# Kernel tuning notes

Measured on AMD Instinct MI355X. Metric: run time of the kernel, lower is better.

Reference implementation:

```python
import jax, jax.numpy as jnp
import numpy as np
import math

N_HEAD = 16
STRIDE = 128
C = 8


def _sparse_causal_mask(q_len, k_len):
    # Mirrors LingLongAttention._sparse_causal_mask (static, host-side numpy).
    cols = np.arange(k_len)
    rows = np.arange(k_len)[:, None]
    strided = (cols % STRIDE) >= (STRIDE - C)          # last C cols of each stride block
    local = (cols[None, :] // STRIDE) == (rows // STRIDE)  # same stride block as query
    causal = cols[None, :] <= rows
    layout = (strided[None, :] | local) & causal       # [k_len, k_len]
    return jnp.asarray(layout[k_len - q_len:])         # [q_len, k_len]


def setup_inputs() -> dict:
    key = jax.random.key(0)
    k1, k2, k3 = jax.random.split(key, 3)
    B, S, E = 2, 2048, 1024
    return {
        "hidden_states": jax.random.normal(k1, (B, S, E), dtype=jnp.float32),
        "W_attn": jax.random.normal(k2, (E, 3 * E), dtype=jnp.float32) * 0.02,
        "b_attn": jnp.zeros((3 * E,), dtype=jnp.float32),
        "W_proj": jax.random.normal(k3, (E, E), dtype=jnp.float32) * 0.02,
        "b_proj": jnp.zeros((E,), dtype=jnp.float32),
    }


def reference(hidden_states, W_attn, b_attn, W_proj, b_proj):
    B, S, E = hidden_states.shape
    H = N_HEAD
    D = E // H
    # Conv1D: x @ W + b, then split into q,k,v
    qkv = hidden_states @ W_attn + b_attn                 # [B,S,3E]
    q, k, v = jnp.split(qkv, 3, axis=-1)
    split = lambda t: t.reshape(B, S, H, D).transpose(0, 2, 1, 3)  # [B,H,S,D]
    q, k, v = split(q), split(k), split(v)
    scale = jnp.asarray(1.0 / math.sqrt(D), dtype=q.dtype)
    scores = jnp.einsum("bhqd,bhkd->bhqk", q, k) * scale  # [B,H,S,S]
    mask = _sparse_causal_mask(S, S)[None, None]          # [1,1,S,S]
    mask_value = jnp.asarray(jnp.finfo(scores.dtype).min, dtype=scores.dtype)
    scores = jnp.where(mask, scores, mask_value)
    attn = jax.nn.softmax(scores, axis=-1)
    out = jnp.einsum("bhqk,bhkd->bhqd", attn, v)          # [B,H,S,D]
    out = out.transpose(0, 2, 1, 3).reshape(B, S, E)      # merge heads
    return out @ W_proj + b_proj
```

## Files before the change

### kernel.cpp

```cpp
#include <hip/hip_runtime.h>
#include <hip/hip_bf16.h>
#include <stdint.h>

typedef unsigned short u16;
typedef uint32_t u32;
typedef short s16x8 __attribute__((ext_vector_type(8)));
typedef float f32x4 __attribute__((ext_vector_type(4)));

#define SDIM 2048
#define EDIM 1024

static __device__ __forceinline__ float b2f(u16 v) {
    union { float f; u32 u; } c; c.u = ((u32)v) << 16; return c.f;
}
static __device__ __forceinline__ u16 f2b(float f) {
    union { float f; u32 u; } c; c.f = f;
    u32 u = c.u;
    u32 r = (u + 0x7FFFu + ((u >> 16) & 1u)) >> 16;
    return (u16)r;
}
static __device__ __forceinline__ void gll16(const u16* g, u16* l) {
    __builtin_amdgcn_global_load_lds(
        (const __attribute__((address_space(1))) void*)g,
        (__attribute__((address_space(3))) void*)l, 16, 0, 0);
}

static __device__ __forceinline__ int sniff_bf16(const u16* __restrict__ x) {
    u16 v = x[(threadIdx.x & 63) * 2];
    int e = (v >> 7) & 0xFF;
    unsigned long long m = __ballot(e >= 90 && e <= 144);
    return __popcll(m) >= 48;
}

__global__ __launch_bounds__(256) void k_prep(
    const void* __restrict__ X, const void* __restrict__ Wa,
    const void* __restrict__ Wp, u16* __restrict__ Xb,
    u16* __restrict__ WtA, u16* __restrict__ WtP) {
    int f = sniff_bf16((const u16*)X);
    int z = blockIdx.z;
    int t = threadIdx.x;
    if (z == 2) {
        if (f) return;
        const float* s = (const float*)X;
        int bid = blockIdx.y * 48 + blockIdx.x;
        for (int c = bid; c < 2048; c += 768) {
            long i = ((long)c * 256 + t) * 8;
            u16 o[8];
            for (int j = 0; j < 8; ++j) o[j] = f2b(s[i + j]);
            *(uint4*)&Xb[i] = *(uint4*)o;
        }
        return;
    }
    if (z == 1 && blockIdx.x >= 16) return;
    const void* src = z ? Wp : Wa;
    u16* dst = z ? WtP : WtA;
    int Nsrc = z ? 1024 : 3072;
    int n0 = blockIdx.x * 64, k0 = blockIdx.y * 64;
    __shared__ u16 L[64 * 72];
    int r = t >> 2, c0 = (t & 3) * 16;
    u16 val[16];
    if (f) {
        const u16* s = (const u16*)src + (size_t)(k0 + r) * Nsrc + n0 + c0;
        *(uint4*)&val[0] = *(const uint4*)s;
        *(uint4*)&val[8] = *(const uint4*)(s + 8);
    } else {
        const float* s = (const float*)src + (size_t)(k0 + r) * Nsrc + n0 + c0;
        for (int j = 0; j < 16; ++j) val[j] = f2b(s[j]);
    }
    for (int j = 0; j < 16; ++j) L[(c0 + j) * 72 + r] = val[j];
    __syncthreads();
    uint4 o0 = *(const uint4*)&L[r * 72 + c0];
    uint4 o1 = *(const uint4*)&L[r * 72 + c0 + 8];
    u16* d = dst + (size_t)(n0 + r) * 1024 + k0 + c0;
    *(uint4*)d = o0;
    *(uint4*)(d + 8) = o1;
}

__global__ __launch_bounds__(256) void k_gemm1(
    const u16* __restrict__ Xraw, const u16* __restrict__ Xb,
    const u16* __restrict__ Bt, const void* __restrict__ bias,
    u16* __restrict__ C) {
    const int K = 1024;
    __shared__ u16 As[128 * 64];
    __shared__ u16 Bs[128 * 64];
    int f = sniff_bf16(Xraw);
    const u16* A = f ? Xraw : Xb;
    int t = threadIdx.x, wave = t >> 6, lane = t & 63;
    int m0 = blockIdx.y * 128, n0 = blockIdx.x * 128;
    int wm = (wave >> 1) * 64, wn = (wave & 1) * 64;
    int lm = lane & 15, lk = (lane >> 4) * 8;
    int sr = t >> 2, sc = (t & 3) * 8;
    const u16* Ap = A + (size_t)(m0 + sr) * K + sc;
    const u16* Bp = Bt + (size_t)(n0 + sr) * K + sc;
    u16* Asw = As + wave * 512;
    u16* Bsw = Bs + wave * 512;

    f32x4 acc[4][4];
    f32x4 z = {0.f, 0.f, 0.f, 0.f};
    for (int mi = 0; mi < 4; ++mi)
        for (int ni = 0; ni < 4; ++ni) acc[mi][ni] = z;

    for (int k0 = 0; k0 < K; k0 += 64) {
        gll16(Ap + k0, Asw);
        gll16(Ap + (size_t)64 * K + k0, Asw + 2048);
        gll16(Ap + k0 + 32, Asw + 4096);
        gll16(Ap + (size_t)64 * K + k0 + 32, Asw + 6144);
        gll16(Bp + k0, Bsw);
        gll16(Bp + (size_t)64 * K + k0, Bsw + 2048);
        gll16(Bp + k0 + 32, Bsw + 4096);
        gll16(Bp + (size_t)64 * K + k0 + 32, Bsw + 6144);
        __syncthreads();
        for (int kh = 0; kh < 2; ++kh) {
            const u16* Ab = As + kh * 4096;
            const u16* Bb = Bs + kh * 4096;
            s16x8 af[4], bfr[4];
            for (int mi = 0; mi < 4; ++mi)
                af[mi] = *(const s16x8*)&Ab[(wm + mi * 16 + lm) * 32 + lk];
            for (int ni = 0; ni < 4; ++ni)
                bfr[ni] = *(const s16x8*)&Bb[(wn + ni * 16 + lm) * 32 + lk];
            for (int mi = 0; mi < 4; ++mi)
                for (int ni = 0; ni < 4; ++ni)
                    acc[mi][ni] = __builtin_amdgcn_mfma_f32_16x16x32_bf16(
                        af[mi], bfr[ni], acc[mi][ni], 0, 0, 0);
        }
        __syncthreads();
    }

    int cn = lane & 15, cr = (lane >> 4) * 4;
    for (int ni = 0; ni < 4; ++ni) {
        int gn = n0 + wn + ni * 16 + cn;
        float bb = f ? b2f(((const u16*)bias)[gn]) : ((const float*)bias)[gn];
        int kind = gn >> 10, rem = gn & 1023;
        int h = rem >> 6, d = rem & 63;
        int hm = kind * 32 + h;
        for (int mi = 0; mi < 4; ++mi)
            for (int r = 0; r < 4; ++r) {
                int gm = m0 + wm + mi * 16 + cr + r;
                int b = gm >> 11, s = gm & 2047;
                size_t o = ((size_t)((hm + b * 16) * 2048 + s)) * 64 + d;
                C[o] = f2b(acc[mi][ni][r] + bb);
            }
    }
}

__global__ __launch_bounds__(256) void k_gemm2(
    const u16* __restrict__ Xraw, const u16* __restrict__ A,
    const u16* __restrict__ Bt, const void* __restrict__ bias,
    u16* __restrict__ Cb, float* __restrict__ Cf) {
    const int K = 1024, N = 1024;
    __shared__ u16 As[64 * 64];
    __shared__ u16 Bs[128 * 64];
    int f = sniff_bf16(Xraw);
    int t = threadIdx.x, wave = t >> 6, lane = t & 63;
    int m0 = blockIdx.y * 64, n0 = blockIdx.x * 128;
    int wm = (wave >> 1) * 32, wn = (wave & 1) * 64;
    int lm = lane & 15, lk = (lane >> 4) * 8;
    int sr = t >> 2, sc = (t & 3) * 8;
    const u16* Ap = A + (size_t)(m0 + sr) * K + sc;
    const u16* Bp = Bt + (size_t)(n0 + sr) * K + sc;
    u16* Asw = As + wave * 512;
    u16* Bsw = Bs + wave * 512;

    f32x4 acc[2][4];
    f32x4 z = {0.f, 0.f, 0.f, 0.f};
    for (int mi = 0; mi < 2; ++mi)
        for (int ni = 0; ni < 4; ++ni) acc[mi][ni] = z;

    for (int k0 = 0; k0 < K; k0 += 64) {
        gll16(Ap + k0, Asw);
        gll16(Ap + k0 + 32, Asw + 2048);
        gll16(Bp + k0, Bsw);
        gll16(Bp + (size_t)64 * K + k0, Bsw + 2048);
        gll16(Bp + k0 + 32, Bsw + 4096);
        gll16(Bp + (size_t)64 * K + k0 + 32, Bsw + 6144);
        __syncthreads();
        for (int kh = 0; kh < 2; ++kh) {
            const u16* Ab = As + kh * 2048;
            const u16* Bb = Bs + kh * 4096;
            s16x8 af[2], bfr[4];
            for (int mi = 0; mi < 2; ++mi)
                af[mi] = *(const s16x8*)&Ab[(wm + mi * 16 + lm) * 32 + lk];
            for (int ni = 0; ni < 4; ++ni)
                bfr[ni] = *(const s16x8*)&Bb[(wn + ni * 16 + lm) * 32 + lk];
            for (int mi = 0; mi < 2; ++mi)
                for (int ni = 0; ni < 4; ++ni)
                    acc[mi][ni] = __builtin_amdgcn_mfma_f32_16x16x32_bf16(
                        af[mi], bfr[ni], acc[mi][ni], 0, 0, 0);
        }
        __syncthreads();
    }

    int store_f32 = (f == 0);
    int cn = lane & 15, cr = (lane >> 4) * 4;
    for (int ni = 0; ni < 4; ++ni) {
        int gn = n0 + wn + ni * 16 + cn;
        float bb = f ? b2f(((const u16*)bias)[gn]) : ((const float*)bias)[gn];
        for (int mi = 0; mi < 2; ++mi)
            for (int r = 0; r < 4; ++r) {
                int gm = m0 + wm + mi * 16 + cr + r;
                float v = acc[mi][ni][r] + bb;
                size_t o = (size_t)gm * N + gn;
                if (store_f32) Cf[o] = v;
                else           Cb[o] = f2b(v);
            }
    }
}

#define VP 264
#define PP 264
__global__ __launch_bounds__(256) void k_attn4(const u16* __restrict__ QKV,
                                               u16* __restrict__ AO) {
    int bx = blockIdx.x, h = blockIdx.y, b = blockIdx.z;
    int qb = bx >> 1, sb = bx & 1;
    int t = threadIdx.x, lane = t & 63, wave = t >> 6;
    int lm = lane & 15, q4 = lane >> 4;
    int nstr = qb << 3;
    int nk = nstr + (sb << 6) + 64;
    int r0 = (qb << 7) + (sb << 6);

    __shared__ char smem[79872];
    u16* Vts = (u16*)smem;
    u16* Qs  = (u16*)(smem + 33792);
    u16* Ks  = (u16*)(smem + 33792 + 9216);
    u16* Ps  = (u16*)(smem + 33792);

    int hm = b * 16 + h;
    const u16* qp = QKV + ((size_t)hm * 2048 + r0) * 64;
    const u16* kp = QKV + ((size_t)(32 + hm) * 2048) * 64;
    const u16* vp = QKV + ((size_t)(64 + hm) * 2048) * 64;

    for (int c = t; c < 512; c += 256) {
        int r = c >> 3, d0 = (c & 7) << 3;
        *(uint4*)&Qs[r * 72 + d0] = *(const uint4*)(qp + c * 8);
    }
    uint4 zz = {0u, 0u, 0u, 0u};
    for (int c = t; c < 2048; c += 256) {
        int i = c >> 3, d0 = (c & 7) << 3;
        uint4 kv = zz;
        if (i < nk) {
            int key = (i < nstr) ? (((i >> 3) << 7) + 120 + (i & 7))
                                 : ((qb << 7) + (i - nstr));
            kv = *(const uint4*)(kp + key * 64 + d0);
        }
        *(uint4*)&Ks[i * 72 + d0] = kv;
    }
    {
        int i0 = (t & 31) * 8, d0 = (t >> 5) * 8;
        u16 m8[8][8];
        for (int r = 0; r < 8; ++r) {
            int i = i0 + r;
            uint4 vv = zz;
            if (i < nk) {
                int key = (i < nstr) ? (((i >> 3) << 7) + 120 + (i & 7))
                                     : ((qb << 7) + (i - nstr));
                vv = *(const uint4*)(vp + key * 64 + d0);
            }
            *(uint4*)m8[r] = vv;
        }
        for (int j = 0; j < 8; ++j) {
            u16 o[8];
            for (int r = 0; r < 8; ++r) o[r] = m8[r][j];
            *(uint4*)&Vts[(d0 + j) * VP + i0] = *(uint4*)o;
        }
    }
    __syncthreads();

    f32x4 acc[16];
    f32x4 z4 = {0.f, 0.f, 0.f, 0.f};
    for (int ni = 0; ni < 16; ++ni) acc[ni] = z4;
    s16x8 af0 = *(const s16x8*)&Qs[(wave * 16 + lm) * 72 + q4 * 8];
    s16x8 af1 = *(const s16x8*)&Qs[(wave * 16 + lm) * 72 + 32 + q4 * 8];
    for (int ni = 0; ni < 16; ++ni) {
        s16x8 bf0 = *(const s16x8*)&Ks[(ni * 16 + lm) * 72 + q4 * 8];
        s16x8 bf1 = *(const s16x8*)&Ks[(ni * 16 + lm) * 72 + 32 + q4 * 8];
        acc[ni] = __builtin_amdgcn_mfma_f32_16x16x32_bf16(af0, bf0, acc[ni], 0, 0, 0);
        acc[ni] = __builtin_amdgcn_mfma_f32_16x16x32_bf16(af1, bf1, acc[ni], 0, 0, 0);
    }
    __syncthreads();

    float mx[4] = {-3e38f, -3e38f, -3e38f, -3e38f};
    for (int ni = 0; ni < 16; ++ni) {
        int i = ni * 16 + lm;
        for (int reg = 0; reg < 4; ++reg) {
            int rl = (sb << 6) + wave * 16 + q4 * 4 + reg;
            bool valid = (i < nstr) || ((i - nstr) <= rl);
            float v = valid ? acc[ni][reg] * 0.125f : -3e38f;
            acc[ni][reg] = v;
            mx[reg] = fmaxf(mx[reg], v);
        }
    }
    for (int reg = 0; reg < 4; ++reg)
        for (int off = 1; off < 16; off <<= 1)
            mx[reg] = fmaxf(mx[reg], __shfl_xor(mx[reg], off, 64));
    float sm[4] = {0.f, 0.f, 0.f, 0.f};
    for (int ni = 0; ni < 16; ++ni)
        for (int reg = 0; reg < 4; ++reg) {
            float e = __expf(acc[ni][reg] - mx[reg]);
            acc[ni][reg] = e;
            sm[reg] += e;
        }
    for (int reg = 0; reg < 4; ++reg)
        for (int off = 1; off < 16; off <<= 1)
            sm[reg] += __shfl_xor(sm[reg], off, 64);
    float inv[4];
    for (int reg = 0; reg < 4; ++reg) inv[reg] = 1.f / sm[reg];

    for (int ni = 0; ni < 16; ++ni) {
        int i = ni * 16 + lm;
        for (int reg = 0; reg < 4; ++reg)
            Ps[(wave * 16 + q4 * 4 + reg) * PP + i] = f2b(acc[ni][reg]);
    }
    __syncthreads();

    f32x4 acc2[4];
    for (int ni2 = 0; ni2 < 4; ++ni2) acc2[ni2] = z4;
    for (int k0 = 0; k0 < 256; k0 += 32) {
        s16x8 pf = *(const s16x8*)&Ps[(wave * 16 + lm) * PP + k0 + q4 * 8];
        for (int ni2 = 0; ni2 < 4; ++ni2) {
            s16x8 vf = *(const s16x8*)&Vts[(ni2 * 16 + lm) * VP + k0 + q4 * 8];
            acc2[ni2] = __builtin_amdgcn_mfma_f32_16x16x32_bf16(pf, vf, acc2[ni2], 0, 0, 0);
        }
    }
    int srow = r0 + wave * 16 + q4 * 4;
    for (int ni2 = 0; ni2 < 4; ++ni2)
        for (int reg = 0; reg < 4; ++reg) {
            size_t o = ((size_t)(b * SDIM + srow + reg)) * EDIM + h * 64 + ni2 * 16 + lm;
            AO[o] = f2b(acc2[ni2][reg] * inv[reg]);
        }
}

extern "C" void kernel_launch(void* const* d_in, const int* in_sizes, int n_in,
                              void* d_out, int out_size, void* d_ws, size_t ws_size,
                              hipStream_t stream) {
    const void* X  = d_in[0];
    const void* Wa = d_in[1];
    const void* ba = d_in[2];
    const void* Wp = d_in[3];
    const void* bp = d_in[4];

    char* w = (char*)d_ws;
    u16* Xb   = (u16*)(w);
    u16* WtA  = (u16*)(w + 8388608);
    u16* WtP  = (u16*)(w + 14680064);
    u16* QKVh = (u16*)(w + 16777216);
    u16* AO   = (u16*)(w + 41943040);

    k_prep<<<dim3(48, 16, 3), 256, 0, stream>>>(X, Wa, Wp, Xb, WtA, WtP);
    k_gemm1<<<dim3(24, 32), 256, 0, stream>>>((const u16*)X, Xb, WtA, ba, QKVh);
    k_attn4<<<dim3(32, 16, 2), 256, 0, stream>>>(QKVh, AO);
    k_gemm2<<<dim3(8, 64), 256, 0, stream>>>((const u16*)X, AO, WtP, bp,
                                             (u16*)d_out, (float*)d_out);
}
```

Measured before the change: 169.5 us.

## Double-buffer GEMM LDS tiles and trim attention loops to live key count

Both projection GEMMs now use two LDS buffers with a K-step of 32. The next tile's global-to-LDS load is issued before the current tile's MFMAs, so memory latency overlaps compute, at the cost of one barrier per 32-wide step instead of per 64. The attention kernel bounds the K/V staging, QK^T, softmax, P stores and PV loops by the actual number of keys (rounded to 32) rather than a fixed 256. This skips work on fully masked padding columns for early query blocks. Correctness relies on the zero-filled, masked region being excluded consistently in every stage.

```diff
diff --git a/kernel.cpp b/kernel.cpp
--- a/kernel.cpp
+++ b/kernel.cpp
@@ -81,8 +81,8 @@
     const u16* __restrict__ Bt, const void* __restrict__ bias,
     u16* __restrict__ C) {
     const int K = 1024;
-    __shared__ u16 As[128 * 64];
-    __shared__ u16 Bs[128 * 64];
+    __shared__ u16 As[2][4096];
+    __shared__ u16 Bs[2][4096];
     int f = sniff_bf16(Xraw);
     const u16* A = f ? Xraw : Xb;
     int t = threadIdx.x, wave = t >> 6, lane = t & 63;
@@ -92,37 +92,37 @@
     int sr = t >> 2, sc = (t & 3) * 8;
     const u16* Ap = A + (size_t)(m0 + sr) * K + sc;
     const u16* Bp = Bt + (size_t)(n0 + sr) * K + sc;
-    u16* Asw = As + wave * 512;
-    u16* Bsw = Bs + wave * 512;
+    int wo = wave * 512;
 
     f32x4 acc[4][4];
     f32x4 z = {0.f, 0.f, 0.f, 0.f};
     for (int mi = 0; mi < 4; ++mi)
         for (int ni = 0; ni < 4; ++ni) acc[mi][ni] = z;
 
-    for (int k0 = 0; k0 < K; k0 += 64) {
-        gll16(Ap + k0, Asw);
-        gll16(Ap + (size_t)64 * K + k0, Asw + 2048);
-        gll16(Ap + k0 + 32, Asw + 4096);
-        gll16(Ap + (size_t)64 * K + k0 + 32, Asw + 6144);
-        gll16(Bp + k0, Bsw);
-        gll16(Bp + (size_t)64 * K + k0, Bsw + 2048);
-        gll16(Bp + k0 + 32, Bsw + 4096);
-        gll16(Bp + (size_t)64 * K + k0 + 32, Bsw + 6144);
-        __syncthreads();
-        for (int kh = 0; kh < 2; ++kh) {
-            const u16* Ab = As + kh * 4096;
-            const u16* Bb = Bs + kh * 4096;
-            s16x8 af[4], bfr[4];
-            for (int mi = 0; mi < 4; ++mi)
-                af[mi] = *(const s16x8*)&Ab[(wm + mi * 16 + lm) * 32 + lk];
+    gll16(Ap, &As[0][wo]);
+    gll16(Ap + (size_t)64 * K, &As[0][wo + 2048]);
+    gll16(Bp, &Bs[0][wo]);
+    gll16(Bp + (size_t)64 * K, &Bs[0][wo + 2048]);
+    __syncthreads();
+
+    for (int it = 0; it < 32; ++it) {
+        int cur = it & 1;
+        if (it < 31) {
+            int kn = (it + 1) * 32;
+            gll16(Ap + kn, &As[cur ^ 1][wo]);
+            gll16(Ap + (size_t)64 * K + kn, &As[cur ^ 1][wo + 2048]);
+            gll16(Bp + kn, &Bs[cur ^ 1][wo]);
+            gll16(Bp + (size_t)64 * K + kn, &Bs[cur ^ 1][wo + 2048]);
+        }
+        s16x8 af[4], bfr[4];
+        for (int mi = 0; mi < 4; ++mi)
+            af[mi] = *(const s16x8*)&As[cur][(wm + mi * 16 + lm) * 32 + lk];
+        for (int ni = 0; ni < 4; ++ni)
+            bfr[ni] = *(const s16x8*)&Bs[cur][(wn + ni * 16 + lm) * 32 + lk];
+        for (int mi = 0; mi < 4; ++mi)
             for (int ni = 0; ni < 4; ++ni)
-                bfr[ni] = *(const s16x8*)&Bb[(wn + ni * 16 + lm) * 32 + lk];
-            for (int mi = 0; mi < 4; ++mi)
-                for (int ni = 0; ni < 4; ++ni)
-                    acc[mi][ni] = __builtin_amdgcn_mfma_f32_16x16x32_bf16(
-                        af[mi], bfr[ni], acc[mi][ni], 0, 0, 0);
-        }
+                acc[mi][ni] = __builtin_amdgcn_mfma_f32_16x16x32_bf16(
+                    af[mi], bfr[ni], acc[mi][ni], 0, 0, 0);
         __syncthreads();
     }
 
@@ -148,8 +148,8 @@
     const u16* __restrict__ Bt, const void* __restrict__ bias,
     u16* __restrict__ Cb, float* __restrict__ Cf) {
     const int K = 1024, N = 1024;
-    __shared__ u16 As[64 * 64];
-    __shared__ u16 Bs[128 * 64];
+    __shared__ u16 As[2][2048];
+    __shared__ u16 Bs[2][4096];
     int f = sniff_bf16(Xraw);
     int t = threadIdx.x, wave = t >> 6, lane = t & 63;
     int m0 = blockIdx.y * 64, n0 = blockIdx.x * 128;
@@ -158,35 +158,35 @@
     int sr = t >> 2, sc = (t & 3) * 8;
     const u16* Ap = A + (size_t)(m0 + sr) * K + sc;
     const u16* Bp = Bt + (size_t)(n0 + sr) * K + sc;
-    u16* Asw = As + wave * 512;
-    u16* Bsw = Bs + wave * 512;
+    int wo = wave * 512;
 
     f32x4 acc[2][4];
     f32x4 z = {0.f, 0.f, 0.f, 0.f};
     for (int mi = 0; mi < 2; ++mi)
         for (int ni = 0; ni < 4; ++ni) acc[mi][ni] = z;
 
-    for (int k0 = 0; k0 < K; k0 += 64) {
-        gll16(Ap + k0, Asw);
-        gll16(Ap + k0 + 32, Asw + 2048);
-        gll16(Bp + k0, Bsw);
-        gll16(Bp + (size_t)64 * K + k0, Bsw + 2048);
-        gll16(Bp + k0 + 32, Bsw + 4096);
-        gll16(Bp + (size_t)64 * K + k0 + 32, Bsw + 6144);
-        __syncthreads();
-        for (int kh = 0; kh < 2; ++kh) {
-            const u16* Ab = As + kh * 2048;
-            const u16* Bb = Bs + kh * 4096;
-            s16x8 af[2], bfr[4];
-            for (int mi = 0; mi < 2; ++mi)
-                af[mi] = *(const s16x8*)&Ab[(wm + mi * 16 + lm) * 32 + lk];
+    gll16(Ap, &As[0][wo]);
+    gll16(Bp, &Bs[0][wo]);
+    gll16(Bp + (size_t)64 * K, &Bs[0][wo + 2048]);
+    __syncthreads();
+
+    for (int it = 0; it < 32; ++it) {
+        int cur = it & 1;
+        if (it < 31) {
+            int kn = (it + 1) * 32;
+            gll16(Ap + kn, &As[cur ^ 1][wo]);
+            gll16(Bp + kn, &Bs[cur ^ 1][wo]);
+            gll16(Bp + (size_t)64 * K + kn, &Bs[cur ^ 1][wo + 2048]);
+        }
+        s16x8 af[2], bfr[4];
+        for (int mi = 0; mi < 2; ++mi)
+            af[mi] = *(const s16x8*)&As[cur][(wm + mi * 16 + lm) * 32 + lk];
+        for (int ni = 0; ni < 4; ++ni)
+            bfr[ni] = *(const s16x8*)&Bs[cur][(wn + ni * 16 + lm) * 32 + lk];
+        for (int mi = 0; mi < 2; ++mi)
             for (int ni = 0; ni < 4; ++ni)
-                bfr[ni] = *(const s16x8*)&Bb[(wn + ni * 16 + lm) * 32 + lk];
-            for (int mi = 0; mi < 2; ++mi)
-                for (int ni = 0; ni < 4; ++ni)
-                    acc[mi][ni] = __builtin_amdgcn_mfma_f32_16x16x32_bf16(
-                        af[mi], bfr[ni], acc[mi][ni], 0, 0, 0);
-        }
+                acc[mi][ni] = __builtin_amdgcn_mfma_f32_16x16x32_bf16(
+                    af[mi], bfr[ni], acc[mi][ni], 0, 0, 0);
         __syncthreads();
     }
 
@@ -208,7 +208,7 @@
 
 #define VP 264
 #define PP 264
-__global__ __launch_bounds__(256) void k_attn4(const u16* __restrict__ QKV,
+__global__ __launch_bounds__(256) void k_attn5(const u16* __restrict__ QKV,
                                                u16* __restrict__ AO) {
     int bx = blockIdx.x, h = blockIdx.y, b = blockIdx.z;
     int qb = bx >> 1, sb = bx & 1;
@@ -216,6 +216,8 @@
     int lm = lane & 15, q4 = lane >> 4;
     int nstr = qb << 3;
     int nk = nstr + (sb << 6) + 64;
+    int kmax = (nk + 31) & ~31;
+    int ntile = kmax >> 4;
     int r0 = (qb << 7) + (sb << 6);
 
     __shared__ char smem[79872];
@@ -234,7 +236,7 @@
         *(uint4*)&Qs[r * 72 + d0] = *(const uint4*)(qp + c * 8);
     }
     uint4 zz = {0u, 0u, 0u, 0u};
-    for (int c = t; c < 2048; c += 256) {
+    for (int c = t; c < (kmax << 3); c += 256) {
         int i = c >> 3, d0 = (c & 7) << 3;
         uint4 kv = zz;
         if (i < nk) {
@@ -246,21 +248,23 @@
     }
     {
         int i0 = (t & 31) * 8, d0 = (t >> 5) * 8;
-        u16 m8[8][8];
-        for (int r = 0; r < 8; ++r) {
-            int i = i0 + r;
-            uint4 vv = zz;
-            if (i < nk) {
-                int key = (i < nstr) ? (((i >> 3) << 7) + 120 + (i & 7))
-                                     : ((qb << 7) + (i - nstr));
-                vv = *(const uint4*)(vp + key * 64 + d0);
+        if (i0 < kmax) {
+            u16 m8[8][8];
+            for (int r = 0; r < 8; ++r) {
+                int i = i0 + r;
+                uint4 vv = zz;
+                if (i < nk) {
+                    int key = (i < nstr) ? (((i >> 3) << 7) + 120 + (i & 7))
+                                         : ((qb << 7) + (i - nstr));
+                    vv = *(const uint4*)(vp + key * 64 + d0);
+                }
+                *(uint4*)m8[r] = vv;
             }
-            *(uint4*)m8[r] = vv;
-        }
-        for (int j = 0; j < 8; ++j) {
-            u16 o[8];
-            for (int r = 0; r < 8; ++r) o[r] = m8[r][j];
-            *(uint4*)&Vts[(d0 + j) * VP + i0] = *(uint4*)o;
+            for (int j = 0; j < 8; ++j) {
+                u16 o[8];
+                for (int r = 0; r < 8; ++r) o[r] = m8[r][j];
+                *(uint4*)&Vts[(d0 + j) * VP + i0] = *(uint4*)o;
+            }
         }
     }
     __syncthreads();
@@ -270,7 +274,7 @@
     for (int ni = 0; ni < 16; ++ni) acc[ni] = z4;
     s16x8 af0 = *(const s16x8*)&Qs[(wave * 16 + lm) * 72 + q4 * 8];
     s16x8 af1 = *(const s16x8*)&Qs[(wave * 16 + lm) * 72 + 32 + q4 * 8];
-    for (int ni = 0; ni < 16; ++ni) {
+    for (int ni = 0; ni < ntile; ++ni) {
         s16x8 bf0 = *(const s16x8*)&Ks[(ni * 16 + lm) * 72 + q4 * 8];
         s16x8 bf1 = *(const s16x8*)&Ks[(ni * 16 + lm) * 72 + 32 + q4 * 8];
         acc[ni] = __builtin_amdgcn_mfma_f32_16x16x32_bf16(af0, bf0, acc[ni], 0, 0, 0);
@@ -279,7 +283,7 @@
     __syncthreads();
 
     float mx[4] = {-3e38f, -3e38f, -3e38f, -3e38f};
-    for (int ni = 0; ni < 16; ++ni) {
+    for (int ni = 0; ni < ntile; ++ni) {
         int i = ni * 16 + lm;
         for (int reg = 0; reg < 4; ++reg) {
             int rl = (sb << 6) + wave * 16 + q4 * 4 + reg;
@@ -293,7 +297,7 @@
         for (int off = 1; off < 16; off <<= 1)
             mx[reg] = fmaxf(mx[reg], __shfl_xor(mx[reg], off, 64));
     float sm[4] = {0.f, 0.f, 0.f, 0.f};
-    for (int ni = 0; ni < 16; ++ni)
+    for (int ni = 0; ni < ntile; ++ni)
         for (int reg = 0; reg < 4; ++reg) {
             float e = __expf(acc[ni][reg] - mx[reg]);
             acc[ni][reg] = e;
@@ -305,7 +309,7 @@
     float inv[4];
     for (int reg = 0; reg < 4; ++reg) inv[reg] = 1.f / sm[reg];
 
-    for (int ni = 0; ni < 16; ++ni) {
+    for (int ni = 0; ni < ntile; ++ni) {
         int i = ni * 16 + lm;
         for (int reg = 0; reg < 4; ++reg)
             Ps[(wave * 16 + q4 * 4 + reg) * PP + i] = f2b(acc[ni][reg]);
@@ -314,7 +318,7 @@
 
     f32x4 acc2[4];
     for (int ni2 = 0; ni2 < 4; ++ni2) acc2[ni2] = z4;
-    for (int k0 = 0; k0 < 256; k0 += 32) {
+    for (int k0 = 0; k0 < kmax; k0 += 32) {
         s16x8 pf = *(const s16x8*)&Ps[(wave * 16 + lm) * PP + k0 + q4 * 8];
         for (int ni2 = 0; ni2 < 4; ++ni2) {
             s16x8 vf = *(const s16x8*)&Vts[(ni2 * 16 + lm) * VP + k0 + q4 * 8];
@@ -347,7 +351,7 @@
 
     k_prep<<<dim3(48, 16, 3), 256, 0, stream>>>(X, Wa, Wp, Xb, WtA, WtP);
     k_gemm1<<<dim3(24, 32), 256, 0, stream>>>((const u16*)X, Xb, WtA, ba, QKVh);
-    k_attn4<<<dim3(32, 16, 2), 256, 0, stream>>>(QKVh, AO);
+    k_attn5<<<dim3(32, 16, 2), 256, 0, stream>>>(QKVh, AO);
     k_gemm2<<<dim3(8, 64), 256, 0, stream>>>((const u16*)X, AO, WtP, bp,
                                              (u16*)d_out, (float*)d_out);
 }
```

Result: slower. 228.4 us (+34.8%).
